# Kernel tuning notes

Measured on AMD Instinct MI355X. Metric: run time of the kernel, lower is better.

## Reference

```python
import jax, jax.numpy as jnp
import numpy as np

B, T, C, H = 2, 2048, 1024, 16
D = C // H  # head_dim = 64


def _ln(x, g, b, eps=1e-5):
    mu = x.mean(-1, keepdims=True)
    var = ((x - mu) ** 2).mean(-1, keepdims=True)
    return (x - mu) / jnp.sqrt(var + eps) * g + b


def _lif_rate(I, tau_rc=0.02, tau_ref=0.002, v_th=1.0, eps=1e-7):
    good = I > v_th + eps
    I_safe = jnp.where(good, I, v_th + 1.0)  # avoid log1p(<=-1)
    r = 1.0 / (tau_ref - tau_rc * jnp.log1p(-v_th / I_safe))
    return jnp.where(good, r, 0.0)


def setup_inputs() -> dict:
    key = jax.random.key(0)
    ks = jax.random.split(key, 12)
    w = lambda k, shp: jax.random.normal(k, shp, dtype=jnp.float32) * 0.02
    enc = jax.random.normal(ks[9], (H, T, D), dtype=jnp.float32)
    enc_hat = enc / jnp.maximum(jnp.linalg.norm(enc, axis=-1, keepdims=True), 1e-8)
    return {
        "x": jax.random.normal(ks[0], (B, T, C), dtype=jnp.float32),
        "ln1_g": jnp.ones((C,), jnp.float32), "ln1_b": jnp.zeros((C,), jnp.float32),
        "qkv_w": w(ks[1], (C, 3 * C)), "qkv_b": jnp.zeros((3 * C,), jnp.float32),
        "out_w": w(ks[2], (C, C)), "out_b": jnp.zeros((C,), jnp.float32),
        "ln2_g": jnp.ones((C,), jnp.float32), "ln2_b": jnp.zeros((C,), jnp.float32),
        "mlp_w1": w(ks[3], (C, 4 * C)), "mlp_b1": jnp.zeros((4 * C,), jnp.float32),
        "mlp_w2": w(ks[4], (4 * C, C)), "mlp_b2": jnp.zeros((C,), jnp.float32),
        "enc_hat": enc_hat,
        "gain": jax.random.uniform(ks[10], (1, H, T, 1), dtype=jnp.float32) * 200.0,
        "bias_attn": jax.random.uniform(ks[11], (1, H, T, 1), dtype=jnp.float32),
    }


def reference(x, ln1_g, ln1_b, qkv_w, qkv_b, out_w, out_b,
              ln2_g, ln2_b, mlp_w1, mlp_b1, mlp_w2, mlp_b2,
              enc_hat, gain, bias_attn):
    b, t, c = x.shape
    x_norm = _ln(x, ln1_g, ln1_b)
    qkv = x_norm @ qkv_w + qkv_b                      # [B,T,3C]
    qkv = qkv.reshape(b, t, 3, H, D).transpose(2, 0, 3, 1, 4)
    Q, K_unused, V = qkv[0], qkv[1], qkv[2]           # each [B,H,T,D]; K unused (matches source)
    E = enc_hat[:, :t, :]
    G = gain[:, :, :t, :]
    BIAS = bias_attn[:, :, :t, :]
    I = G * jnp.einsum('bhtd,hsd->bhts', Q, E) + BIAS  # [B,H,T,T]
    scores = _lif_rate(I) / jnp.sqrt(jnp.float32(D))
    causal = jnp.tril(jnp.ones((t, t), dtype=bool))[None, None]
    scores = jnp.where(causal, scores, -jnp.inf)
    attn_w = jax.nn.softmax(scores, axis=-1)
    attn_out = jnp.einsum('bhts,bhsd->bhtd', attn_w, V)
    attn_out = attn_out.transpose(0, 2, 1, 3).reshape(b, t, c)
    x = x + attn_out @ out_w + out_b
    h = _ln(x, ln2_g, ln2_b)
    h = jax.nn.gelu(h @ mlp_w1 + mlp_b1, approximate=False) @ mlp_w2 + mlp_b2
    return x + h
```

## Files before the change

kernel.cpp:

```cpp
#include <hip/hip_runtime.h>
#include <math.h>

#define Bdim 2
#define Tdim 2048
#define Cdim 1024
#define Hdim 16
#define Ddim 64

typedef unsigned short u16;
typedef __attribute__((ext_vector_type(8))) short bf16x8;
typedef __attribute__((ext_vector_type(4))) float f32x4;

__device__ __forceinline__ float b2f(u16 s){
  union { float f; unsigned u; } v; v.u = ((unsigned)s) << 16; return v.f;
}
__device__ __forceinline__ u16 f2b(float f){
  union { float f; unsigned u; } v; v.f = f;
  unsigned r = v.u + 0x7fffu + ((v.u >> 16) & 1u);
  return (u16)(r >> 16);
}
__device__ __forceinline__ float loadf(const void* p, size_t i, int bf){
  float r;
  if(bf) r = b2f(((const u16*)p)[i]);
  else   r = ((const float*)p)[i];
  return r;
}
__device__ __forceinline__ f32x4 mfma16(bf16x8 a, bf16x8 b, f32x4 c){
  return __builtin_amdgcn_mfma_f32_16x16x32_bf16(a, b, c, 0, 0, 0);
}
__device__ __forceinline__ void glds16(const u16* g, u16* l){
  __builtin_amdgcn_global_load_lds(
      (const __attribute__((address_space(1))) unsigned int*)g,
      (__attribute__((address_space(3))) unsigned int*)l, 16, 0, 0);
}

__global__ void detect_k(const u16* __restrict__ x, int* __restrict__ flag){
  if(threadIdx.x == 0 && blockIdx.x == 0){
    int sane = 0;
    for(int i = 0; i < 64; i++){
      int e = (x[i] >> 7) & 0xFF;
      sane += (e == 0 || (e >= 0x6E && e <= 0x8A)) ? 1 : 0;
    }
    *flag = (sane >= 56) ? 1 : 0;
  }
}

__global__ __launch_bounds__(256) void cvt_k(const void* __restrict__ in,
    u16* __restrict__ out, int n, const int* __restrict__ flagp){
  int bf = *flagp;
  int i = blockIdx.x * 256 + threadIdx.x;
  if(i < n) out[i] = bf ? ((const u16*)in)[i] : f2b(((const float*)in)[i]);
}

__global__ __launch_bounds__(256) void transpose_k(const void* __restrict__ in,
    u16* __restrict__ out, int K, int N, const int* __restrict__ flagp){
  __shared__ u16 tile[32][34];
  int bf = *flagp;
  int n0 = blockIdx.x * 32, k0 = blockIdx.y * 32;
  int tx = threadIdx.x & 31, ty = threadIdx.x >> 5;
  #pragma unroll
  for(int i = 0; i < 4; i++)
    tile[ty + i*8][tx] = f2b(loadf(in, (size_t)(k0 + ty + i*8) * N + n0 + tx, bf));
  __syncthreads();
  #pragma unroll
  for(int i = 0; i < 4; i++)
    out[(size_t)(n0 + ty + i*8) * K + k0 + tx] = tile[tx][ty + i*8];
}

template<int SRC>
__global__ __launch_bounds__(256) void ln_k(const void* __restrict__ xin,
    const void* __restrict__ g, const void* __restrict__ be,
    u16* __restrict__ out, const int* __restrict__ flagp){
  __shared__ float red[256];
  int bf = *flagp;
  int row = blockIdx.x, t = threadIdx.x;
  float v[4]; float s = 0.f;
  #pragma unroll
  for(int i = 0; i < 4; i++){
    size_t idx = (size_t)row * Cdim + t + i*256;
    v[i] = (SRC == 1) ? ((const float*)xin)[idx] : loadf(xin, idx, bf);
    s += v[i];
  }
  red[t] = s; __syncthreads();
  for(int o = 128; o > 0; o >>= 1){ if(t < o) red[t] += red[t+o]; __syncthreads(); }
  float mu = red[0] * (1.f / Cdim);
  __syncthreads();
  s = 0.f;
  #pragma unroll
  for(int i = 0; i < 4; i++){ float d = v[i] - mu; s += d*d; }
  red[t] = s; __syncthreads();
  for(int o = 128; o > 0; o >>= 1){ if(t < o) red[t] += red[t+o]; __syncthreads(); }
  float rstd = rsqrtf(red[0] * (1.f / Cdim) + 1e-5f);
  u16* orow = out + (size_t)row * Cdim;
  #pragma unroll
  for(int i = 0; i < 4; i++){
    int c = t + i*256;
    orow[c] = f2b((v[i] - mu) * rstd * loadf(g, c, bf) + loadf(be, c, bf));
  }
}

enum { EPI_QKV = 0, EPI_RES = 1, EPI_GELU = 2, EPI_FINAL = 3 };

template<int EPI, int KK, int MODE>
__global__ __launch_bounds__(256) void gemm_k(
    const u16* __restrict__ A, const u16* __restrict__ Bt, const void* __restrict__ bias,
    void* __restrict__ out0, void* __restrict__ out1, const void* __restrict__ res,
    int M, int N, int mofs, const int* __restrict__ flagp)
{
  const int K = KK;
  const int BK    = (MODE == 2) ? 128 : 64;
  const int TILEU = 128 * BK;
  __shared__ u16 As[(MODE == 2 ? 2 : 1) * 128 * ((MODE == 2) ? 128 : 64)];
  __shared__ u16 Bs[(MODE == 2 ? 2 : 1) * 128 * ((MODE == 2) ? 128 : 64)];
  int bf = *flagp;
  int tid = threadIdx.x;
  int nblk = (int)(gridDim.x * gridDim.y);
  int orig = (int)(blockIdx.y * gridDim.x + blockIdx.x);
  int wgid = (orig & 7) * (nblk >> 3) + (orig >> 3);
  int bx = wgid % (int)gridDim.x, by = wgid / (int)gridDim.x;
  int m0 = by * 128, n0 = bx * 128;
  int w = tid >> 6, l = tid & 63;
  int lq = l & 15, lk = l >> 4;
  int m_off = (w & 1) * 64, n_off = (w >> 1) * 64;
  const u16* Bbase = Bt +
      (size_t)(n0 + ((EPI == EPI_QKV && n0 >= 1024) ? 1024 : 0)) * K;
  const u16* Abase = A + (size_t)m0 * K;
  int grow = w * 32 + (l >> 3);
  int gcol = (((l & 7) ^ ((l >> 3) & 7))) * 8;
  const u16* Ab0 = Abase + (size_t)grow * K + gcol;
  const u16* Bb0 = Bbase + (size_t)grow * K + gcol;

  #define STAGE64(buf, k0)                                                  \
    do{ _Pragma("unroll")                                                   \
      for(int i = 0; i < 4; i++)                                            \
        glds16(Ab0 + (size_t)(i*8) * K + (k0),                              \
               &As[(buf)*TILEU + (w*32 + i*8) * 64]);                       \
      _Pragma("unroll")                                                     \
      for(int i = 0; i < 4; i++)                                            \
        glds16(Bb0 + (size_t)(i*8) * K + (k0),                              \
               &Bs[(buf)*TILEU + (w*32 + i*8) * 64]);                       \
    } while(0)

  #define STAGE128(buf, k0)                                                 \
    do{ _Pragma("unroll")                                                   \
      for(int i = 0; i < 8; i++){                                           \
        int rr = i*4 + (l >> 4);                                            \
        int cc = ((l & 15) ^ ((rr + w*32) & 15)) * 8;                       \
        glds16(Abase + (size_t)(w*32 + rr) * K + (k0) + cc,                 \
               &As[(buf)*TILEU + (w*32 + i*4) * 128]);                      \
        glds16(Bbase + (size_t)(w*32 + rr) * K + (k0) + cc,                 \
               &Bs[(buf)*TILEU + (w*32 + i*4) * 128]);                      \
      }                                                                     \
    } while(0)

  #define STAGE(buf, k0)                                                    \
    do{ if(MODE == 2) STAGE128(buf, k0); else STAGE64(buf, k0); } while(0)

  f32x4 acc[4][4] = {};
  #define COMPUTE(buf)                                                         \
    do{ _Pragma("unroll")                                                      \
      for(int kk = 0; kk < (MODE == 2 ? 4 : 2); kk++){                         \
        bf16x8 af[4], bfr[4];                                                  \
        _Pragma("unroll")                                                      \
        for(int mb = 0; mb < 4; mb++)                                          \
          af[mb]  = *(const bf16x8*)&As[(buf)*TILEU +                          \
              (m_off + mb*16 + lq) * BK + (((kk*4 + lk) ^ (lq & (BK/8 - 1))) * 8)]; \
        _Pragma("unroll")                                                      \
        for(int nb = 0; nb < 4; nb++)                                          \
          bfr[nb] = *(const bf16x8*)&Bs[(buf)*TILEU +                          \
              (n_off + nb*16 + lq) * BK + (((kk*4 + lk) ^ (lq & (BK/8 - 1))) * 8)]; \
        _Pragma("unroll")                                                      \
        for(int mb = 0; mb < 4; mb++)                                          \
          _Pragma("unroll")                                                    \
          for(int nb = 0; nb < 4; nb++)                                        \
            acc[mb][nb] = mfma16(af[mb], bfr[nb], acc[mb][nb]);                \
      }                                                                        \
    } while(0)

  if(MODE == 2){
    int cur = 0;
    STAGE(0, 0);
    __syncthreads();
    for(int k0 = 0; k0 < K; k0 += BK){
      if(k0 + BK < K) STAGE(cur ^ 1, k0 + BK);
      COMPUTE(cur);
      __syncthreads();
      cur ^= 1;
    }
  } else {
    for(int k0 = 0; k0 < K; k0 += 64){
      __syncthreads();
      STAGE64(0, k0);
      __syncthreads();
      COMPUTE(0);
    }
  }
  #undef STAGE64
  #undef STAGE128
  #undef STAGE
  #undef COMPUTE

  #pragma unroll
  for(int mb = 0; mb < 4; mb++)
  #pragma unroll
  for(int nb = 0; nb < 4; nb++){
    #pragma unroll
    for(int r = 0; r < 4; r++){
      int m = m0 + m_off + mb*16 + lk*4 + r;
      int n = n0 + n_off + nb*16 + lq;
      float v = acc[mb][nb][r];
      if(EPI == EPI_QKV){
        int bsrc = (n < 1024) ? n : n + 1024;
        v += loadf(bias, bsrc, bf);
        int bb = m / Tdim, t = m % Tdim;
        if(n < 1024){
          int h = n >> 6, d = n & 63;
          ((u16*)out0)[(((size_t)(bb*Hdim + h)*Tdim + t) << 6) + d] = f2b(v);
        } else {
          int nv = n - 1024; int h = nv >> 6, d = nv & 63;
          ((u16*)out1)[((size_t)(bb*Hdim + h)*Ddim + d)*Tdim + t] = f2b(v);
        }
      } else if(EPI == EPI_RES){
        v += loadf(bias, n, bf) + loadf(res, (size_t)m*N + n, bf);
        ((float*)out0)[(size_t)m*N + n] = v;
      } else if(EPI == EPI_GELU){
        v += loadf(bias, n, bf);
        float gl = 0.5f * v * (1.0f + erff(v * 0.70710678118f));
        ((u16*)out0)[(size_t)m*N + n] = f2b(gl);
      } else {
        v += loadf(bias, n, bf) + ((const float*)res)[(size_t)m*N + n];
        size_t oi = (size_t)(mofs + m) * N + n;
        if(bf) ((u16*)out0)[oi] = f2b(v);
        else   ((float*)out0)[oi] = v;
      }
    }
  }
}

__global__ __launch_bounds__(256, 3) void attn_k(
    const u16* __restrict__ Q, const u16* __restrict__ Vt, const u16* __restrict__ E,
    const void* __restrict__ gain, const void* __restrict__ battn,
    u16* __restrict__ aout, const int* __restrict__ flagp)
{
  __shared__ u16 Es[2][64][72];
  __shared__ u16 Vs[2][64][72];
  __shared__ u16 P[4][16][72];
  int bf = *flagp;
  int k  = 31 - (int)(blockIdx.x >> 5);
  int bh = blockIdx.x & 31;
  int b = bh >> 4, h = bh & 15;
  int tid = threadIdx.x;
  int w = tid >> 6, l = tid & 63;
  int lq = l & 15, lk = l >> 4;
  int rt = k * 4 + w;
  int qrow = rt * 16;
  const u16* Qb = Q  + (size_t)bh * Tdim * Ddim;
  const u16* Vb = Vt + (size_t)bh * Ddim * Tdim;
  const u16* Eh = E  + (size_t)h  * Tdim * Ddim;
  int srow = tid >> 3;
  int scol = (tid & 7) * 8;
  bf16x8 qf[2];
  #pragma unroll
  for(int ks = 0; ks < 2; ks++)
    qf[ks] = *(const bf16x8*)(Qb + (size_t)(qrow + lq) * Ddim + ks*32 + lk*8);
  float g4[4], b4[4];
  #pragma unroll
  for(int r = 0; r < 4; r++){
    int t = qrow + lk*4 + r;
    g4[r] = loadf(gain, h * Tdim + t, bf);
    b4[r] = loadf(battn, h * Tdim + t, bf);
  }
  bf16x8 onesf;
  #pragma unroll
  for(int j = 0; j < 8; j++) onesf[j] = (short)0x3F80;
  f32x4 num[4] = {};
  f32x4 den4 = {0.f, 0.f, 0.f, 0.f};
  {
    bf16x8 e0 = *(const bf16x8*)(Eh + (size_t)(srow     ) * Ddim + scol);
    bf16x8 e1 = *(const bf16x8*)(Eh + (size_t)(srow + 32) * Ddim + scol);
    bf16x8 v0 = *(const bf16x8*)(Vb + (size_t)(srow     ) * Tdim + scol);
    bf16x8 v1 = *(const bf16x8*)(Vb + (size_t)(srow + 32) * Tdim + scol);
    *(bf16x8*)&Es[0][srow     ][scol] = e0;
    *(bf16x8*)&Es[0][srow + 32][scol] = e1;
    *(bf16x8*)&Vs[0][srow     ][scol] = v0;
    *(bf16x8*)&Vs[0][srow + 32][scol] = v1;
  }
  __syncthreads();
  for(int st = 0; st <= k; st++){
    int cur = st & 1;
    bf16x8 pe0, pe1, pv0, pv1;
    if(st < k){
      pe0 = *(const bf16x8*)(Eh + (size_t)((st+1)*64 + srow     ) * Ddim + scol);
      pe1 = *(const bf16x8*)(Eh + (size_t)((st+1)*64 + srow + 32) * Ddim + scol);
      pv0 = *(const bf16x8*)(Vb + (size_t)(srow     ) * Tdim + (st+1)*64 + scol);
      pv1 = *(const bf16x8*)(Vb + (size_t)(srow + 32) * Tdim + (st+1)*64 + scol);
    }
    f32x4 sc[4] = {};
    __builtin_amdgcn_s_setprio(1);
    #pragma unroll
    for(int ks = 0; ks < 2; ks++){
      #pragma unroll
      for(int nb = 0; nb < 4; nb++){
        bf16x8 ef = *(const bf16x8*)&Es[cur][nb*16 + lq][ks*32 + lk*8];
        sc[nb] = mfma16(qf[ks], ef, sc[nb]);
      }
    }
    __builtin_amdgcn_s_setprio(0);
    int diag = (st == k);
    #pragma unroll
    for(int nb = 0; nb < 4; nb++){
      #pragma unroll
      for(int r = 0; r < 4; r++){
        int sg = st*64 + nb*16 + lq;
        int qg = qrow + lk*4 + r;
        float I = fmaf(g4[r], sc[nb][r], b4[r]);
        float u = (I - 1.0f) * __builtin_amdgcn_rcpf(I);
        float L = __builtin_amdgcn_logf(u);
        float denom = fmaf(-0.013862944f, L, 0.002f);
        float e = __builtin_amdgcn_exp2f(0.18033688f * __builtin_amdgcn_rcpf(denom));
        float p = (I > 1.0000001f) ? e : 1.0f;
        if(diag) p = (sg <= qg) ? p : 0.f;
        P[w][lk*4 + r][nb*16 + lq] = f2b(p);
      }
    }
    __builtin_amdgcn_s_setprio(1);
    #pragma unroll
    for(int ks = 0; ks < 2; ks++){
      bf16x8 pf = *(const bf16x8*)&P[w][lq][ks*32 + lk*8];
      den4 = mfma16(pf, onesf, den4);
      #pragma unroll
      for(int nb = 0; nb < 4; nb++){
        bf16x8 vf = *(const bf16x8*)&Vs[cur][nb*16 + lq][ks*32 + lk*8];
        num[nb] = mfma16(pf, vf, num[nb]);
      }
    }
    __builtin_amdgcn_s_setprio(0);
    if(st < k){
      *(bf16x8*)&Es[cur^1][srow     ][scol] = pe0;
      *(bf16x8*)&Es[cur^1][srow + 32][scol] = pe1;
      *(bf16x8*)&Vs[cur^1][srow     ][scol] = pv0;
      *(bf16x8*)&Vs[cur^1][srow + 32][scol] = pv1;
      __syncthreads();
    }
  }
  float rden[4];
  #pragma unroll
  for(int r = 0; r < 4; r++) rden[r] = __builtin_amdgcn_rcpf(den4[r]);
  #pragma unroll
  for(int nb = 0; nb < 4; nb++){
    #pragma unroll
    for(int r = 0; r < 4; r++){
      int t = qrow + lk*4 + r;
      int d = nb*16 + lq;
      float o = num[nb][r] * rden[r];
      aout[((size_t)b * Tdim + t) * Cdim + h * Ddim + d] = f2b(o);
    }
  }
}

extern "C" void kernel_launch(void* const* d_in, const int* in_sizes, int n_in,
                              void* d_out, int out_size, void* d_ws, size_t ws_size,
                              hipStream_t stream)
{
  const void* x      = d_in[0];
  const void* ln1_g  = d_in[1];
  const void* ln1_b  = d_in[2];
  const void* qkv_w  = d_in[3];
  const void* qkv_b  = d_in[4];
  const void* out_w  = d_in[5];
  const void* out_b  = d_in[6];
  const void* ln2_g  = d_in[7];
  const void* ln2_b  = d_in[8];
  const void* mlp_w1 = d_in[9];
  const void* mlp_b1 = d_in[10];
  const void* mlp_w2 = d_in[11];
  const void* mlp_b2 = d_in[12];
  const void* enc    = d_in[13];
  const void* gain   = d_in[14];
  const void* battn  = d_in[15];
  (void)in_sizes; (void)n_in; (void)out_size;

  const size_t MB = 1024 * 1024;
  char* ws = (char*)d_ws;
  int*   flag = (int*)(ws);
  u16*   R0   = (u16*)(ws + 256);
  u16*   R1   = (u16*)(ws + 256 + 8*MB);
  float* x2   = (float*)(ws + 256 + 16*MB);
  u16*   R3a  = (u16*)(ws + 256 + 32*MB);
  u16*   R3b  = (u16*)(ws + 256 + 40*MB);
  u16*   Ebf  = (u16*)(ws + 256 + 48*MB);
  u16*   gbuf = (u16*)(ws + 256 + 52*MB);
  bool fullM = ws_size >= 85*MB;

  dim3 blk(256);
  detect_k<<<1, 64, 0, stream>>>((const u16*)x, flag);
  ln_k<0><<<4096, blk, 0, stream>>>(x, ln1_g, ln1_b, R0, flag);
  transpose_k<<<dim3(3072/32, 1024/32), blk, 0, stream>>>(qkv_w, R1, 1024, 3072, flag);
  cvt_k<<<(Hdim*Tdim*Ddim)/256, blk, 0, stream>>>(enc, Ebf, Hdim*Tdim*Ddim, flag);
  gemm_k<EPI_QKV,1024,0><<<dim3(2048/128, 4096/128), blk, 0, stream>>>(
      R0, R1, qkv_b, R3a, R3b, nullptr, 4096, 2048, 0, flag);
  attn_k<<<dim3(32*32), dim3(256), 0, stream>>>(R3a, R3b, Ebf, gain, battn, R0, flag);
  transpose_k<<<dim3(1024/32, 1024/32), blk, 0, stream>>>(out_w, R1, 1024, 1024, flag);
  gemm_k<EPI_RES,1024,2><<<dim3(1024/128, 4096/128), blk, 0, stream>>>(
      R0, R1, out_b, x2, nullptr, x, 4096, 1024, 0, flag);
  ln_k<1><<<4096, blk, 0, stream>>>(x2, ln2_g, ln2_b, R3a, flag);
  transpose_k<<<dim3(4096/32, 1024/32), blk, 0, stream>>>(mlp_w1, R0, 1024, 4096, flag);
  transpose_k<<<dim3(1024/32, 4096/32), blk, 0, stream>>>(mlp_w2, R1, 4096, 1024, flag);
  if(fullM){
    gemm_k<EPI_GELU,1024,0><<<dim3(4096/128, 4096/128), blk, 0, stream>>>(
        R3a, R0, mlp_b1, gbuf, nullptr, nullptr, 4096, 4096, 0, flag);
    gemm_k<EPI_FINAL,4096,2><<<dim3(1024/128, 4096/128), blk, 0, stream>>>(
        gbuf, R1, mlp_b2, d_out, nullptr, x2, 4096, 1024, 0, flag);
  } else {
    for(int q = 0; q < 4; q++){
      int ro = q * 1024;
      gemm_k<EPI_GELU,1024,2><<<dim3(4096/128, 1024/128), blk, 0, stream>>>(
          R3a + (size_t)ro*1024, R0, mlp_b1, R3b, nullptr, nullptr, 1024, 4096, 0, flag);
      gemm_k<EPI_FINAL,4096,2><<<dim3(1024/128, 1024/128), blk, 0, stream>>>(
          R3b, R1, mlp_b2, d_out, nullptr, x2 + (size_t)ro*1024, 1024, 1024, ro, flag);
    }
  }
}
```

Measured before the change: 445.8 us.

## Add 256x256-tile, 512-thread double-buffered GEMM mode for MLP up-projection

Adds a MODE 4 GEMM variant with 256x256 output tiles, 8 waves of 512 threads, BK=64 and double-buffered LDS staging, each wave computing a 128x64 sub-tile. The fullM MLP first GEMM (GELU epilogue) now uses it instead of the single-buffered 128x128 mode. The larger tile raises data reuse per global load and overlaps loads with MFMA work. The costs are more accumulator registers per thread, 128 KB of LDS per block for the shared arrays, and only 256 blocks in the grid, which may lower occupancy.

```diff
diff --git a/kernel.cpp b/kernel.cpp
--- a/kernel.cpp
+++ b/kernel.cpp
@@ -102,31 +102,34 @@
 enum { EPI_QKV = 0, EPI_RES = 1, EPI_GELU = 2, EPI_FINAL = 3 };
 
 template<int EPI, int KK, int MODE>
-__global__ __launch_bounds__(256) void gemm_k(
+__global__ __launch_bounds__(MODE == 4 ? 512 : 256) void gemm_k(
     const u16* __restrict__ A, const u16* __restrict__ Bt, const void* __restrict__ bias,
     void* __restrict__ out0, void* __restrict__ out1, const void* __restrict__ res,
     int M, int N, int mofs, const int* __restrict__ flagp)
 {
   const int K = KK;
   const int BK    = (MODE == 2) ? 128 : 64;
-  const int TILEU = 128 * BK;
-  __shared__ u16 As[(MODE == 2 ? 2 : 1) * 128 * ((MODE == 2) ? 128 : 64)];
-  __shared__ u16 Bs[(MODE == 2 ? 2 : 1) * 128 * ((MODE == 2) ? 128 : 64)];
+  const int BM    = (MODE == 4) ? 256 : 128;
+  const int TILEU = BM * BK;
+  const int MBf   = (MODE == 4) ? 8 : 4;
+  __shared__ u16 As[(MODE >= 2) ? 32768 : 8192];
+  __shared__ u16 Bs[(MODE >= 2) ? 32768 : 8192];
   int bf = *flagp;
   int tid = threadIdx.x;
   int nblk = (int)(gridDim.x * gridDim.y);
   int orig = (int)(blockIdx.y * gridDim.x + blockIdx.x);
   int wgid = (orig & 7) * (nblk >> 3) + (orig >> 3);
   int bx = wgid % (int)gridDim.x, by = wgid / (int)gridDim.x;
-  int m0 = by * 128, n0 = bx * 128;
+  int m0 = by * BM, n0 = bx * BM;
   int w = tid >> 6, l = tid & 63;
   int lq = l & 15, lk = l >> 4;
-  int m_off = (w & 1) * 64, n_off = (w >> 1) * 64;
+  int m_off = (MODE == 4) ? (w >> 2) * 128 : (w & 1) * 64;
+  int n_off = (MODE == 4) ? (w & 3) * 64  : (w >> 1) * 64;
   const u16* Bbase = Bt +
       (size_t)(n0 + ((EPI == EPI_QKV && n0 >= 1024) ? 1024 : 0)) * K;
   const u16* Abase = A + (size_t)m0 * K;
-  int grow = w * 32 + (l >> 3);
   int gcol = (((l & 7) ^ ((l >> 3) & 7))) * 8;
+  int grow = ((MODE == 4) ? w * 8 : w * 32) + (l >> 3);
   const u16* Ab0 = Abase + (size_t)grow * K + gcol;
   const u16* Bb0 = Bbase + (size_t)grow * K + gcol;
 
@@ -139,6 +142,16 @@
       for(int i = 0; i < 4; i++)                                            \
         glds16(Bb0 + (size_t)(i*8) * K + (k0),                              \
                &Bs[(buf)*TILEU + (w*32 + i*8) * 64]);                       \
+    } while(0)
+
+  #define STAGE256(buf, k0)                                                 \
+    do{ _Pragma("unroll")                                                   \
+      for(int i = 0; i < 4; i++){                                           \
+        glds16(Ab0 + (size_t)(i*64) * K + (k0),                             \
+               &As[(buf)*TILEU + (i*64 + w*8) * 64]);                       \
+        glds16(Bb0 + (size_t)(i*64) * K + (k0),                             \
+               &Bs[(buf)*TILEU + (i*64 + w*8) * 64]);                       \
+      }                                                                     \
     } while(0)
 
   #define STAGE128(buf, k0)                                                 \
@@ -154,15 +167,17 @@
     } while(0)
 
   #define STAGE(buf, k0)                                                    \
-    do{ if(MODE == 2) STAGE128(buf, k0); else STAGE64(buf, k0); } while(0)
-
-  f32x4 acc[4][4] = {};
+    do{ if(MODE == 2) STAGE128(buf, k0);                                    \
+        else if(MODE == 4) STAGE256(buf, k0);                               \
+        else STAGE64(buf, k0); } while(0)
+
+  f32x4 acc[MBf][4] = {};
   #define COMPUTE(buf)                                                         \
     do{ _Pragma("unroll")                                                      \
       for(int kk = 0; kk < (MODE == 2 ? 4 : 2); kk++){                         \
-        bf16x8 af[4], bfr[4];                                                  \
+        bf16x8 af[MBf], bfr[4];                                                \
         _Pragma("unroll")                                                      \
-        for(int mb = 0; mb < 4; mb++)                                          \
+        for(int mb = 0; mb < MBf; mb++)                                        \
           af[mb]  = *(const bf16x8*)&As[(buf)*TILEU +                          \
               (m_off + mb*16 + lq) * BK + (((kk*4 + lk) ^ (lq & (BK/8 - 1))) * 8)]; \
         _Pragma("unroll")                                                      \
@@ -170,14 +185,14 @@
           bfr[nb] = *(const bf16x8*)&Bs[(buf)*TILEU +                          \
               (n_off + nb*16 + lq) * BK + (((kk*4 + lk) ^ (lq & (BK/8 - 1))) * 8)]; \
         _Pragma("unroll")                                                      \
-        for(int mb = 0; mb < 4; mb++)                                          \
+        for(int mb = 0; mb < MBf; mb++)                                        \
           _Pragma("unroll")                                                    \
           for(int nb = 0; nb < 4; nb++)                                        \
             acc[mb][nb] = mfma16(af[mb], bfr[nb], acc[mb][nb]);                \
       }                                                                        \
     } while(0)
 
-  if(MODE == 2){
+  if(MODE == 2 || MODE == 4){
     int cur = 0;
     STAGE(0, 0);
     __syncthreads();
@@ -197,11 +212,12 @@
   }
   #undef STAGE64
   #undef STAGE128
+  #undef STAGE256
   #undef STAGE
   #undef COMPUTE
 
   #pragma unroll
-  for(int mb = 0; mb < 4; mb++)
+  for(int mb = 0; mb < MBf; mb++)
   #pragma unroll
   for(int nb = 0; nb < 4; nb++){
     #pragma unroll
@@ -407,7 +423,7 @@
   transpose_k<<<dim3(4096/32, 1024/32), blk, 0, stream>>>(mlp_w1, R0, 1024, 4096, flag);
   transpose_k<<<dim3(1024/32, 4096/32), blk, 0, stream>>>(mlp_w2, R1, 4096, 1024, flag);
   if(fullM){
-    gemm_k<EPI_GELU,1024,0><<<dim3(4096/128, 4096/128), blk, 0, stream>>>(
+    gemm_k<EPI_GELU,1024,4><<<dim3(4096/256, 4096/256), dim3(512), 0, stream>>>(
         R3a, R0, mlp_b1, gbuf, nullptr, nullptr, 4096, 4096, 0, flag);
     gemm_k<EPI_FINAL,4096,2><<<dim3(1024/128, 4096/128), blk, 0, stream>>>(
         gbuf, R1, mlp_b2, d_out, nullptr, x2, 4096, 1024, 0, flag);
```

Measured after the change: 558.9 us. +25.4%, slower.
